# Optimization experiments

Hardware: AMD Instinct MI355X
Metric: run time of the kernel (lower is better)

The kernel has to match this reference:

```python
import jax, jax.numpy as jnp
import numpy as np
from jax import lax

HEADS = 4
NEG_SLOPE = 0.2


def _layernorm(x, g, b, eps=1e-5):
    m = x.mean(-1, keepdims=True)
    v = ((x - m) ** 2).mean(-1, keepdims=True)
    return (x - m) * lax.rsqrt(v + eps) * g + b


def setup_inputs() -> dict:
    key = jax.random.key(0)
    ks = jax.random.split(key, 10)
    B, N, T, H, E, ED, K = 1, 1000, 32, 128, 16000, 16, 3
    s_h = 1.0 / np.sqrt(H)
    s_e = 1.0 / np.sqrt(ED)
    return {
        "x": jax.random.normal(ks[0], (B, N, T, H), jnp.float32),
        "edge_index": jax.random.randint(ks[1], (2, E), 0, N, dtype=jnp.int32),
        "edge_attr": jax.random.normal(ks[2], (E, ED), jnp.float32),
        "conv_w": jax.random.normal(ks[3], (H, H, K), jnp.float32) * (1.0 / np.sqrt(H * K)),
        "conv_b": jnp.zeros((H,), jnp.float32),
        "ln1_g": jnp.ones((H,), jnp.float32),
        "ln1_b": jnp.zeros((H,), jnp.float32),
        "Wl": jax.random.normal(ks[4], (H, H), jnp.float32) * s_h,
        "Wr": jax.random.normal(ks[5], (H, H), jnp.float32) * s_h,
        "We": jax.random.normal(ks[6], (ED, H), jnp.float32) * s_e,
        "att": jax.random.normal(ks[7], (HEADS, H // HEADS), jnp.float32) * s_h,
        "gat_b": jnp.zeros((H,), jnp.float32),
        "ln2_g": jnp.ones((H,), jnp.float32),
        "ln2_b": jnp.zeros((H,), jnp.float32),
    }


def reference(x, edge_index, edge_attr, conv_w, conv_b, ln1_g, ln1_b,
              Wl, Wr, We, att, gat_b, ln2_g, ln2_b):
    B, N, T, H = x.shape
    K = HEADS
    D = H // K
    E = edge_attr.shape[0]

    # ---- temporal sub-block: per-node Conv1d over time ('same' padding) ----
    xt = x.reshape(B * N, T, H).transpose(0, 2, 1)            # [BN, H, T]
    y = lax.conv_general_dilated(xt, conv_w, (1,), 'SAME',
                                 dimension_numbers=('NCH', 'OIH', 'NCH'))
    y = y + conv_b[None, :, None]
    y = y.transpose(0, 2, 1).reshape(B, N, T, H)
    x = _layernorm(x + y, ln1_g, ln1_b)

    # ---- spatial sub-block: GATv2 at every timestep (mega-batch of G graphs) ----
    G = B * T
    xs = x.transpose(0, 2, 1, 3).reshape(G, N, H)             # [G, N, H]

    # add self-loops, fill_value='mean' (mean of incoming edge attrs per node)
    dst0 = edge_index[1]
    cnt = jax.ops.segment_sum(jnp.ones((E,), edge_attr.dtype), dst0, num_segments=N)
    loop_attr = jax.ops.segment_sum(edge_attr, dst0, num_segments=N) / jnp.maximum(cnt, 1.0)[:, None]
    ea = jnp.concatenate([edge_attr, loop_attr], axis=0)       # [E+N, ED]
    loops = jnp.arange(N, dtype=edge_index.dtype)
    src = jnp.concatenate([edge_index[0], loops])
    dst = jnp.concatenate([edge_index[1], loops])

    gl = jnp.einsum('gnh,hkd->gnkd', xs, Wl.reshape(H, K, D))  # source transform
    gr = jnp.einsum('gnh,hkd->gnkd', xs, Wr.reshape(H, K, D))  # target transform
    ee = jnp.einsum('ef,fkd->ekd', ea, We.reshape(-1, K, D))   # edge transform

    e_src = jnp.swapaxes(gl[:, src], 0, 1)                     # [E', G, K, D]
    e_dst = jnp.swapaxes(gr[:, dst], 0, 1)                     # [E', G, K, D]
    s = jax.nn.leaky_relu(e_src + e_dst + ee[:, None], NEG_SLOPE)
    logits = jnp.einsum('egkd,kd->egk', s, att)                # [E', G, K]

    # scatter-softmax over incoming edges per target node (self-loops => non-empty)
    mx = jax.ops.segment_max(logits, dst, num_segments=N)[dst]
    ex = jnp.exp(logits - mx)
    den = jax.ops.segment_sum(ex, dst, num_segments=N)[dst]
    alpha = ex / den

    aggr = jax.ops.segment_sum(e_src * alpha[..., None], dst, num_segments=N)  # [N, G, K, D]
    out = jnp.swapaxes(aggr, 0, 1).reshape(G, N, H) + gat_b

    out = out.reshape(B, T, N, H).transpose(0, 2, 1, 3)        # back to (B, N, T, H)
    return _layernorm(x + out, ln2_g, ln2_b)
```

## Files before the change

kernel.cpp:

```cpp
#include <hip/hip_runtime.h>
#include <math.h>

#define N_NODES 1000
#define T_STEPS 32
#define H_DIM   128
#define E_EDGES 16000
#define ED_DIM  16
#define G_GRAPHS 32
#define EP_EDGES (E_EDGES + N_NODES)
#define NEG_SLOPE 0.2f
#define LN_EPS 1e-5f
#define CSR_CAP 128

typedef __attribute__((ext_vector_type(8))) short bf16x8;
typedef __attribute__((ext_vector_type(16))) float f32x16;
typedef __attribute__((ext_vector_type(4))) float f32x4;
typedef __attribute__((ext_vector_type(4))) unsigned u32x4;
typedef unsigned short u16;

__device__ inline short f2bf(float f) {
    unsigned u = __float_as_uint(f);
    u = (u + 0x7FFFu + ((u >> 16) & 1u)) >> 16;
    return (short)u;
}
__device__ inline float bf2f(u16 u) { return __uint_as_float(((unsigned)u) << 16); }
__device__ inline float bflo(unsigned u) { return __uint_as_float(u << 16); }
__device__ inline float bfhi(unsigned u) { return __uint_as_float(u & 0xFFFF0000u); }

__global__ __launch_bounds__(1024) void k_prep(
    const float* __restrict__ conv_w, const float* __restrict__ Wl,
    const float* __restrict__ Wr, short* __restrict__ wc, short* __restrict__ wg) {
    int i = blockIdx.x * 1024 + threadIdx.x;
    if (i < 4 * 24 * 64 * 8) {
        int r = i & 7, lane = (i >> 3) & 63;
        int t = i >> 9;
        int kstep = t % 24, ct = t / 24;
        int k = kstep >> 3, hs = kstep & 7;
        int hi = hs * 16 + ((lane >> 5) << 3) + r;
        int o = ct * 32 + (lane & 31);
        wc[i] = f2bf(conv_w[(o * H_DIM + hi) * 3 + k]);
    } else {
        int j = i - 4 * 24 * 64 * 8;
        int r = j & 7, lane = (j >> 3) & 63;
        int ks = (j >> 9) & 7, ct = j >> 12;
        int hi = ks * 16 + ((lane >> 5) << 3) + r;
        int o = ct * 32 + (lane & 31);
        wg[j] = f2bf(o < H_DIM ? Wl[hi * H_DIM + o] : Wr[hi * H_DIM + o - H_DIM]);
    }
}

__global__ __launch_bounds__(256) void k_fuse(
    const float* __restrict__ x, const short* __restrict__ wc, const short* __restrict__ wg,
    const float* __restrict__ conv_b, const float* __restrict__ ln1_g,
    const float* __restrict__ ln1_b, const float* __restrict__ edge_attr,
    const float* __restrict__ We, const int* __restrict__ dst,
    int* __restrict__ csr, int* __restrict__ cnt,
    u16* __restrict__ x1b, u16* __restrict__ gl, u16* __restrict__ gr,
    u16* __restrict__ ee) {
    __shared__ __align__(16) short xb[34 * 136];
    __shared__ __align__(16) float yb[32 * 136];
    __shared__ int buf[CSR_CAP];
    __shared__ float laf[16];
    __shared__ int scnt;
    int b = blockIdx.x;
    int tid = threadIdx.x;

    if (b >= 2000) {
        int e0 = (b - 2000) * 16 + (tid >> 7);
        int h = tid & 127;
#pragma unroll
        for (int k = 0; k < 16; k += 2) {
            int e = e0 + k;
            const float* ea = &edge_attr[e * ED_DIM];
            float acc = 0.f;
#pragma unroll
            for (int f = 0; f < ED_DIM; ++f) acc += ea[f] * We[f * H_DIM + h];
            __builtin_nontemporal_store((u16)f2bf(acc), &ee[(size_t)e * H_DIM + h]);
        }
        return;
    }
    if (b >= 1000) {
        int n = b - 1000;
        if (tid == 0) scnt = 0;
        __syncthreads();
        const uint4* d4 = (const uint4*)dst;
        for (int i = tid; i < E_EDGES / 4; i += 256) {
            uint4 v = d4[i];
            int e0 = i * 4;
            if ((int)v.x == n) { int s = atomicAdd(&scnt, 1); if (s < CSR_CAP) buf[s] = e0; }
            if ((int)v.y == n) { int s = atomicAdd(&scnt, 1); if (s < CSR_CAP) buf[s] = e0 + 1; }
            if ((int)v.z == n) { int s = atomicAdd(&scnt, 1); if (s < CSR_CAP) buf[s] = e0 + 2; }
            if ((int)v.w == n) { int s = atomicAdd(&scnt, 1); if (s < CSR_CAP) buf[s] = e0 + 3; }
        }
        __syncthreads();
        int deg = min(scnt, CSR_CAP);
        if (tid == 0) cnt[n] = deg;
        bool fast = (deg <= 64);
        if (fast) {
            if (tid < 64) {
                int v = (tid < deg) ? buf[tid] : 0x7FFFFFFF;
                int rank = 0;
#pragma unroll
                for (int j = 0; j < 64; ++j) {
                    int vj = __shfl(v, j);
                    rank += (vj < v) ? 1 : 0;
                }
                if (tid < deg) buf[rank] = v;
            }
        } else {
            if (tid == 0) {
                for (int i = 1; i < deg; ++i) {
                    int key = buf[i], j = i - 1;
                    while (j >= 0 && buf[j] > key) { buf[j + 1] = buf[j]; --j; }
                    buf[j + 1] = key;
                }
            }
        }
        __syncthreads();
        if (tid < deg) csr[n * CSR_CAP + tid] = buf[tid];
        if (tid < 64) {
            int q = tid >> 4, f = tid & 15;
            float a = 0.f;
            for (int i = q; i < deg; i += 4) a += edge_attr[buf[i] * ED_DIM + f];
            a += __shfl_xor(a, 16);
            a += __shfl_xor(a, 32);
            if (tid < 16) laf[tid] = a / fmaxf((float)deg, 1.0f);
        }
        __syncthreads();
        if (tid < H_DIM) {
            float acc = 0.f;
#pragma unroll
            for (int f = 0; f < ED_DIM; ++f) acc += laf[f] * We[f * H_DIM + tid];
            ee[(size_t)(E_EDGES + n) * H_DIM + tid] = (u16)f2bf(acc);
        }
        return;
    }

    int n = b;
    int w = tid >> 6, lane = tid & 63;
    int arow = lane & 31;
    int aks = (lane >> 5) << 3;

    {
        const f32x4* xs4 = (const f32x4*)(x + (size_t)n * T_STEPS * H_DIM);
        for (int i4 = tid; i4 < T_STEPS * H_DIM / 4; i4 += 256) {
            f32x4 v = __builtin_nontemporal_load(&xs4[i4]);
            int t = i4 >> 5, h = (i4 * 4) & 127;
            uint2 pp;
            pp.x = (unsigned)(unsigned short)f2bf(v.x) | ((unsigned)(unsigned short)f2bf(v.y) << 16);
            pp.y = (unsigned)(unsigned short)f2bf(v.z) | ((unsigned)(unsigned short)f2bf(v.w) << 16);
            *(uint2*)&xb[(t + 1) * 136 + h] = pp;
        }
        if (tid < 68) {
            ((unsigned*)xb)[tid] = 0u;
            ((unsigned*)(xb + 33 * 136))[tid] = 0u;
        }
    }
    __syncthreads();

    f32x16 acc = {};
    for (int kk = 0; kk < 3; ++kk) {
#pragma unroll
        for (int hs = 0; hs < 8; ++hs) {
            int kstep = kk * 8 + hs;
            bf16x8 a = *(const bf16x8*)&xb[(arow + kk) * 136 + hs * 16 + aks];
            bf16x8 bb = *(const bf16x8*)&wc[((w * 24 + kstep) * 64 + lane) * 8];
            acc = __builtin_amdgcn_mfma_f32_32x32x16_bf16(a, bb, acc, 0, 0, 0);
        }
    }
    {
        int oc = w * 32 + (lane & 31);
        float cb = conv_b[oc];
#pragma unroll
        for (int r = 0; r < 16; ++r) {
            int t = (r & 3) + 8 * (r >> 2) + 4 * (lane >> 5);
            yb[t * 136 + oc] = acc[r] + cb;
        }
    }
    __syncthreads();

    float rr0[8], rr1[8];
#pragma unroll
    for (int idx = 0; idx < 8; ++idx) {
        int t = w + idx * 4;
        rr0[idx] = bf2f((u16)xb[(t + 1) * 136 + lane]) + yb[t * 136 + lane];
        rr1[idx] = bf2f((u16)xb[(t + 1) * 136 + lane + 64]) + yb[t * 136 + lane + 64];
    }
    __syncthreads();
    float g0c = ln1_g[lane], g1c = ln1_g[lane + 64];
    float b0c = ln1_b[lane], b1c = ln1_b[lane + 64];
#pragma unroll
    for (int idx = 0; idx < 8; ++idx) {
        int t = w + idx * 4;
        float r0 = rr0[idx], r1 = rr1[idx];
        float s = r0 + r1, s2 = r0 * r0 + r1 * r1;
#pragma unroll
        for (int mm = 1; mm < 64; mm <<= 1) {
            s += __shfl_xor(s, mm);
            s2 += __shfl_xor(s2, mm);
        }
        float mean = s * (1.f / 128.f);
        float var = s2 * (1.f / 128.f) - mean * mean;
        float rs = rsqrtf(var + LN_EPS);
        float o0 = (r0 - mean) * rs * g0c + b0c;
        float o1 = (r1 - mean) * rs * g1c + b1c;
        xb[t * 136 + lane] = f2bf(o0);
        xb[t * 136 + lane + 64] = f2bf(o1);
    }
    __syncthreads();

    for (int c = tid; c < 512; c += 256) {
        int t = c >> 4, p = c & 15;
        u32x4 v = *(const u32x4*)&xb[t * 136 + p * 8];
        *(u32x4*)&x1b[((size_t)n * T_STEPS + t) * H_DIM + p * 8] = v;
    }

    f32x16 cl = {}, cr = {};
#pragma unroll
    for (int ks = 0; ks < 8; ++ks) {
        bf16x8 a = *(const bf16x8*)&xb[arow * 136 + ks * 16 + aks];
        bf16x8 b0 = *(const bf16x8*)&wg[(((2 * w) * 8 + ks) * 64 + lane) * 8];
        bf16x8 b1 = *(const bf16x8*)&wg[(((2 * w + 1) * 8 + ks) * 64 + lane) * 8];
        cl = __builtin_amdgcn_mfma_f32_32x32x16_bf16(a, b0, cl, 0, 0, 0);
        cr = __builtin_amdgcn_mfma_f32_32x32x16_bf16(a, b1, cr, 0, 0, 0);
    }
    __syncthreads();
    {
        u16* st = (u16*)yb;
        int m = w >> 1;
        int c0 = (w & 1) * 64 + (lane & 31);
#pragma unroll
        for (int r = 0; r < 16; ++r) {
            int t = (r & 3) + 8 * (r >> 2) + 4 * (lane >> 5);
            st[(m * 32 + t) * 136 + c0] = (u16)f2bf(cl[r]);
            st[(m * 32 + t) * 136 + c0 + 32] = (u16)f2bf(cr[r]);
        }
    }
    __syncthreads();
    {
        const u16* st = (const u16*)yb;
        for (int c = tid; c < 1024; c += 256) {
            int m = c >> 9, t = (c >> 4) & 31, p = c & 15;
            u32x4 v = *(const u32x4*)&st[(m * 32 + t) * 136 + p * 8];
            u16* d = m ? gr : gl;
            *(u32x4*)&d[((size_t)t * N_NODES + n) * H_DIM + p * 8] = v;
        }
    }
}

__global__ __launch_bounds__(128) void k_gat(
    const u16* __restrict__ gl, const u16* __restrict__ gr, const u16* __restrict__ ee,
    const int* __restrict__ src_arr, const int* __restrict__ csr,
    const int* __restrict__ cnt, const float* __restrict__ att,
    const float* __restrict__ gat_b, const u16* __restrict__ x1b,
    const float* __restrict__ ln2_g, const float* __restrict__ ln2_b,
    float* __restrict__ out) {
    int bid = blockIdx.x;
    int q = bid & 3;
    int n = bid >> 2;
    int tid = threadIdx.x;
    int gs = tid >> 4;
    int r = tid & 15;
    int h0 = ((r >> 2) << 5) + ((r & 3) << 3);
    int g = q + 4 * gs;

    __shared__ int es[64], ss[64];
    int off = n * CSR_CAP, deg = cnt[n];
    int tot = deg + 1;

    float av[8], grv[8];
    {
        float4 a0 = *(const float4*)&att[h0];
        float4 a1 = *(const float4*)&att[h0 + 4];
        av[0] = a0.x; av[1] = a0.y; av[2] = a0.z; av[3] = a0.w;
        av[4] = a1.x; av[5] = a1.y; av[6] = a1.z; av[7] = a1.w;
        u32x4 g4 = *(const u32x4*)&gr[((size_t)g * N_NODES + n) * H_DIM + h0];
        grv[0] = bflo(g4.x); grv[1] = bfhi(g4.x); grv[2] = bflo(g4.y); grv[3] = bfhi(g4.y);
        grv[4] = bflo(g4.z); grv[5] = bfhi(g4.z); grv[6] = bflo(g4.w); grv[7] = bfhi(g4.w);
    }
    const u16* glg = gl + (size_t)g * N_NODES * H_DIM + h0;
    const u16* eeh = ee + h0;

    size_t ob = ((size_t)n * T_STEPS + g) * H_DIM + h0;
    u32x4 xv = __builtin_nontemporal_load((const u32x4*)&x1b[ob]);

    float m = -INFINITY, l = 0.f;
    float ac[8] = {0.f, 0.f, 0.f, 0.f, 0.f, 0.f, 0.f, 0.f};

    auto LDQ = [&](u32x4& G, u32x4& E, int idx) {
        int s_ = ss[idx], e_ = es[idx];
        G = *(const u32x4*)&glg[(size_t)s_ * H_DIM];
        E = __builtin_nontemporal_load((const u32x4*)&eeh[(size_t)e_ * H_DIM]);
    };
    auto PROC = [&](u32x4 gc, u32x4 ec) {
        float gvv[8];
        gvv[0] = bflo(gc.x); gvv[1] = bfhi(gc.x); gvv[2] = bflo(gc.y); gvv[3] = bfhi(gc.y);
        gvv[4] = bflo(gc.z); gvv[5] = bfhi(gc.z); gvv[6] = bflo(gc.w); gvv[7] = bfhi(gc.w);
        float evv[8];
        evv[0] = bflo(ec.x); evv[1] = bfhi(ec.x); evv[2] = bflo(ec.y); evv[3] = bfhi(ec.y);
        evv[4] = bflo(ec.z); evv[5] = bfhi(ec.z); evv[6] = bflo(ec.w); evv[7] = bfhi(ec.w);
        float p = 0.f;
#pragma unroll
        for (int j = 0; j < 8; ++j) {
            float sf = gvv[j] + grv[j] + evv[j];
            sf = fmaxf(sf, NEG_SLOPE * sf);
            p = fmaf(sf, av[j], p);
        }
        p += __shfl_xor(p, 1);
        p += __shfl_xor(p, 2);
        float mn = fmaxf(m, p);
        float sc = __expf(m - mn);
        float wq = __expf(p - mn);
        l = l * sc + wq;
#pragma unroll
        for (int j = 0; j < 8; ++j) ac[j] = ac[j] * sc + wq * gvv[j];
        m = mn;
    };

    for (int base = 0; base < tot; base += 64) {
        int c = min(64, tot - base);
        __syncthreads();
        if (tid < c) {
            int i = base + tid;
            int e = (i < deg) ? csr[off + i] : (E_EDGES + n);
            es[tid] = e;
            ss[tid] = (i < deg) ? src_arr[e] : n;
        }
        __syncthreads();
        int c1 = c - 1;
        u32x4 gA, eA, gB, eB, gC, eC, gD, eD;
        LDQ(gA, eA, 0);
        LDQ(gB, eB, min(1, c1));
        LDQ(gC, eC, min(2, c1));
        LDQ(gD, eD, min(3, c1));
        for (int i = 0; i < c; i += 4) {
            u32x4 g0 = gA, e0 = eA, g1 = gB, e1 = eB;
            u32x4 g2 = gC, e2 = eC, g3 = gD, e3 = eD;
            LDQ(gA, eA, min(i + 4, c1));
            LDQ(gB, eB, min(i + 5, c1));
            LDQ(gC, eC, min(i + 6, c1));
            LDQ(gD, eD, min(i + 7, c1));
            PROC(g0, e0);
            if (i + 1 < c) PROC(g1, e1);
            if (i + 2 < c) PROC(g2, e2);
            if (i + 3 < c) PROC(g3, e3);
        }
    }

    float linv = 1.0f / l;
    float4 gb0 = *(const float4*)&gat_b[h0];
    float4 gb1 = *(const float4*)&gat_b[h0 + 4];
    float xr[8];
    xr[0] = bflo(xv.x); xr[1] = bfhi(xv.x); xr[2] = bflo(xv.y); xr[3] = bfhi(xv.y);
    xr[4] = bflo(xv.z); xr[5] = bfhi(xv.z); xr[6] = bflo(xv.w); xr[7] = bfhi(xv.w);
    float gbv[8] = {gb0.x, gb0.y, gb0.z, gb0.w, gb1.x, gb1.y, gb1.z, gb1.w};
    float rv[8];
    float s1 = 0.f, s2v = 0.f;
#pragma unroll
    for (int j = 0; j < 8; ++j) {
        rv[j] = xr[j] + ac[j] * linv + gbv[j];
        s1 += rv[j];
        s2v += rv[j] * rv[j];
    }
#pragma unroll
    for (int mm = 1; mm < 16; mm <<= 1) {
        s1 += __shfl_xor(s1, mm);
        s2v += __shfl_xor(s2v, mm);
    }
    float mean = s1 * (1.f / 128.f);
    float var = s2v * (1.f / 128.f) - mean * mean;
    float rs = rsqrtf(var + LN_EPS);
    float4 g20 = *(const float4*)&ln2_g[h0];
    float4 g21 = *(const float4*)&ln2_g[h0 + 4];
    float4 b20 = *(const float4*)&ln2_b[h0];
    float4 b21 = *(const float4*)&ln2_b[h0 + 4];
    f32x4 o0, o1;
    o0.x = (rv[0] - mean) * rs * g20.x + b20.x;
    o0.y = (rv[1] - mean) * rs * g20.y + b20.y;
    o0.z = (rv[2] - mean) * rs * g20.z + b20.z;
    o0.w = (rv[3] - mean) * rs * g20.w + b20.w;
    o1.x = (rv[4] - mean) * rs * g21.x + b21.x;
    o1.y = (rv[5] - mean) * rs * g21.y + b21.y;
    o1.z = (rv[6] - mean) * rs * g21.z + b21.z;
    o1.w = (rv[7] - mean) * rs * g21.w + b21.w;
    __builtin_nontemporal_store(o0, (f32x4*)&out[ob]);
    __builtin_nontemporal_store(o1, (f32x4*)&out[ob + 4]);
}

extern "C" void kernel_launch(void* const* d_in, const int* in_sizes, int n_in,
                              void* d_out, int out_size, void* d_ws, size_t ws_size,
                              hipStream_t stream) {
    const float* x         = (const float*)d_in[0];
    const int*   ei        = (const int*)d_in[1];
    const float* edge_attr = (const float*)d_in[2];
    const float* conv_w    = (const float*)d_in[3];
    const float* conv_b    = (const float*)d_in[4];
    const float* ln1_g     = (const float*)d_in[5];
    const float* ln1_b     = (const float*)d_in[6];
    const float* Wl        = (const float*)d_in[7];
    const float* Wr        = (const float*)d_in[8];
    const float* We        = (const float*)d_in[9];
    const float* att       = (const float*)d_in[10];
    const float* gat_b     = (const float*)d_in[11];
    const float* ln2_g     = (const float*)d_in[12];
    const float* ln2_b     = (const float*)d_in[13];
    float* out = (float*)d_out;

    const int* src = ei;
    const int* dst = ei + E_EDGES;

    u16* x1b    = (u16*)d_ws;
    u16* glb    = x1b + 4096000;
    u16* grb    = glb + 4096000;
    u16* eeb    = grb + 4096000;
    int* cnt    = (int*)(eeb + 2176000);
    int* csr    = cnt + 1000;
    short* wc   = (short*)(csr + 128000);
    short* wg   = wc + 49152;

    k_prep<<<80, 1024, 0, stream>>>(conv_w, Wl, Wr, wc, wg);
    k_fuse<<<3000, 256, 0, stream>>>(x, wc, wg, conv_b, ln1_g, ln1_b, edge_attr, We,
                                     dst, csr, cnt, x1b, glb, grb, eeb);
    k_gat<<<4 * N_NODES, 128, 0, stream>>>(glb, grb, eeb, src, csr, cnt,
                                           att, gat_b, x1b, ln2_g, ln2_b, out);
}
```

Before: 72.98 us.

## Shrink LDS staging buffer to bf16 and add lazy online-softmax rescaling

```diff
diff --git a/kernel.cpp b/kernel.cpp
--- a/kernel.cpp
+++ b/kernel.cpp
@@ -58,7 +58,7 @@
     u16* __restrict__ x1b, u16* __restrict__ gl, u16* __restrict__ gr,
     u16* __restrict__ ee) {
     __shared__ __align__(16) short xb[34 * 136];
-    __shared__ __align__(16) float yb[32 * 136];
+    __shared__ __align__(16) u16 yb[32 * 136];
     __shared__ int buf[CSR_CAP];
     __shared__ float laf[16];
     __shared__ int scnt;
@@ -174,7 +174,7 @@
 #pragma unroll
         for (int r = 0; r < 16; ++r) {
             int t = (r & 3) + 8 * (r >> 2) + 4 * (lane >> 5);
-            yb[t * 136 + oc] = acc[r] + cb;
+            yb[t * 136 + oc] = (u16)f2bf(acc[r] + cb);
         }
     }
     __syncthreads();
@@ -183,8 +183,8 @@
 #pragma unroll
     for (int idx = 0; idx < 8; ++idx) {
         int t = w + idx * 4;
-        rr0[idx] = bf2f((u16)xb[(t + 1) * 136 + lane]) + yb[t * 136 + lane];
-        rr1[idx] = bf2f((u16)xb[(t + 1) * 136 + lane + 64]) + yb[t * 136 + lane + 64];
+        rr0[idx] = bf2f((u16)xb[(t + 1) * 136 + lane]) + bf2f(yb[t * 136 + lane]);
+        rr1[idx] = bf2f((u16)xb[(t + 1) * 136 + lane + 64]) + bf2f(yb[t * 136 + lane + 64]);
     }
     __syncthreads();
     float g0c = ln1_g[lane], g1c = ln1_g[lane + 64];
@@ -225,26 +225,25 @@
         cr = __builtin_amdgcn_mfma_f32_32x32x16_bf16(a, b1, cr, 0, 0, 0);
     }
     __syncthreads();
-    {
-        u16* st = (u16*)yb;
-        int m = w >> 1;
-        int c0 = (w & 1) * 64 + (lane & 31);
-#pragma unroll
-        for (int r = 0; r < 16; ++r) {
-            int t = (r & 3) + 8 * (r >> 2) + 4 * (lane >> 5);
-            st[(m * 32 + t) * 136 + c0] = (u16)f2bf(cl[r]);
-            st[(m * 32 + t) * 136 + c0 + 32] = (u16)f2bf(cr[r]);
-        }
-    }
-    __syncthreads();
-    {
-        const u16* st = (const u16*)yb;
-        for (int c = tid; c < 1024; c += 256) {
-            int m = c >> 9, t = (c >> 4) & 31, p = c & 15;
-            u32x4 v = *(const u32x4*)&st[(m * 32 + t) * 136 + p * 8];
-            u16* d = m ? gr : gl;
+#pragma unroll
+    for (int m = 0; m < 2; ++m) {
+        if ((w >> 1) == m) {
+            int c0 = (w & 1) * 64 + (lane & 31);
+#pragma unroll
+            for (int r = 0; r < 16; ++r) {
+                int t = (r & 3) + 8 * (r >> 2) + 4 * (lane >> 5);
+                yb[t * 136 + c0] = (u16)f2bf(cl[r]);
+                yb[t * 136 + c0 + 32] = (u16)f2bf(cr[r]);
+            }
+        }
+        __syncthreads();
+        u16* d = m ? gr : gl;
+        for (int c = tid; c < 512; c += 256) {
+            int t = c >> 4, p = c & 15;
+            u32x4 v = *(const u32x4*)&yb[t * 136 + p * 8];
             *(u32x4*)&d[((size_t)t * N_NODES + n) * H_DIM + p * 8] = v;
         }
+        __syncthreads();
     }
 }
 
@@ -308,13 +307,21 @@
         }
         p += __shfl_xor(p, 1);
         p += __shfl_xor(p, 2);
-        float mn = fmaxf(m, p);
-        float sc = __expf(m - mn);
-        float wq = __expf(p - mn);
-        l = l * sc + wq;
-#pragma unroll
-        for (int j = 0; j < 8; ++j) ac[j] = ac[j] * sc + wq * gvv[j];
-        m = mn;
+        bool grow = p > m + 8.f;
+        if (__any(grow)) {
+            float mn = fmaxf(m, p);
+            float sc = __expf(m - mn);
+            float wq = __expf(p - mn);
+            l = l * sc + wq;
+#pragma unroll
+            for (int j = 0; j < 8; ++j) ac[j] = ac[j] * sc + wq * gvv[j];
+            m = mn;
+        } else {
+            float wq = __expf(p - m);
+            l += wq;
+#pragma unroll
+            for (int j = 0; j < 8; ++j) ac[j] = fmaf(wq, gvv[j], ac[j]);
+        }
     };
 
     for (int base = 0; base < tot; base += 64) {
```

Measured after the change: 76.26 us. 4.5% more time.
